# Performance work log

Measured on AMD Instinct MI355X. Metric: run time of the kernel, lower is better.

Reference implementation:

```python
import jax, jax.numpy as jnp
import numpy as np

B, C_IN, C_OUT, H, W, K = 8, 64, 64, 128, 128, 3
KK = K * K


def _conv(x, w, b):
    # 3x3, stride 1, padding 1 (matches nn.Conv2d(stride=1, padding=1))
    y = jax.lax.conv_general_dilated(
        x, w, window_strides=(1, 1), padding=((1, 1), (1, 1)),
        dimension_numbers=('NCHW', 'OIHW', 'NCHW'))
    return y + b[None, :, None, None]


def setup_inputs() -> dict:
    key = jax.random.key(0)
    k1, k2, k3, k4, k5 = jax.random.split(key, 5)
    x = jax.random.normal(k1, (B, C_IN, H, W), jnp.float32)
    s = 1.0 / np.sqrt(C_IN * K * K)  # torch conv default init range
    w_off = jax.random.uniform(k2, (2 * KK, C_IN, K, K), jnp.float32, -s, s)
    b_off = jax.random.uniform(k3, (2 * KK,), jnp.float32, -s, s)
    w_reg = jax.random.uniform(k4, (C_OUT, C_IN, K, K), jnp.float32, -s, s)
    b_reg = jax.random.uniform(k5, (C_OUT,), jnp.float32, -s, s)
    return {"x": x, "w_off": w_off, "b_off": b_off, "w_reg": w_reg, "b_reg": b_reg}


def _deform_sample(x, offsets):
    # Equivalent of the K*K grid_sample(align_corners=True, padding_mode='zeros')
    # loop + sum over kernel positions. The norm/unnorm cancel, so sampling is
    # at absolute pixel coords base_grid + offsets.
    B_, C, H_, W_ = x.shape
    off = offsets.reshape(B_, KK, 2, H_, W_).transpose(0, 3, 4, 1, 2)  # B,H,W,KK,2
    xs = off[..., 0] + jnp.arange(W_, dtype=x.dtype)[None, None, :, None]
    ys = off[..., 1] + jnp.arange(H_, dtype=x.dtype)[None, :, None, None]
    x0 = jnp.floor(xs)
    y0 = jnp.floor(ys)
    wx1 = xs - x0
    wx0 = 1.0 - wx1
    wy1 = ys - y0
    wy0 = 1.0 - wy1
    x_flat = x.reshape(B_, C, H_ * W_)

    def gather(yi, xi, w):
        valid = (xi >= 0) & (xi < W_) & (yi >= 0) & (yi < H_)  # zeros padding
        xi_c = jnp.clip(xi, 0, W_ - 1).astype(jnp.int32)
        yi_c = jnp.clip(yi, 0, H_ - 1).astype(jnp.int32)
        idx = (yi_c * W_ + xi_c).reshape(B_, 1, H_ * W_ * KK)
        g = jnp.take_along_axis(
            x_flat, jnp.broadcast_to(idx, (B_, C, H_ * W_ * KK)), axis=2)
        g = g.reshape(B_, C, H_, W_, KK)
        wm = (w * valid.astype(x.dtype))[:, None]  # B,1,H,W,KK
        return (g * wm).sum(-1)  # sum over the KK kernel positions

    return (gather(y0, x0, wy0 * wx0)
            + gather(y0, x0 + 1.0, wy0 * wx1)
            + gather(y0 + 1.0, x0, wy1 * wx0)
            + gather(y0 + 1.0, x0 + 1.0, wy1 * wx1))


def reference(x, w_off, b_off, w_reg, b_reg):
    offsets = _conv(x, w_off, b_off)          # B, 2*KK, H, W
    sampled = _deform_sample(x, offsets)      # B, C, H, W (summed over KK)
    return _conv(sampled, w_reg, b_reg)       # B, C_OUT, H, W
```

## Files before the change

### kernel.cpp

```cpp
#include <hip/hip_runtime.h>

#define B_ 8
#define CIN 64
#define COUT 64
#define H_ 128
#define W_ 128
#define HW (H_*W_)
#define OFFP 24

typedef __attribute__((ext_vector_type(8))) short short8;
typedef __attribute__((ext_vector_type(4))) short s16x4;
typedef __attribute__((ext_vector_type(4))) float f32x4;
typedef __attribute__((ext_vector_type(2))) float f32x2;

__device__ __forceinline__ short f2bf(float f) {
    unsigned u = __float_as_uint(f);
    unsigned r = (u + 0x7fffu + ((u >> 16) & 1u)) >> 16;
    return (short)r;
}
__device__ __forceinline__ float bf2f(short s) {
    return __uint_as_float(((unsigned)(unsigned short)s) << 16);
}

template<int NT>
__device__ __forceinline__ void prep_one(const float* __restrict__ w, short* __restrict__ o,
                                         int i, int n_used) {
    int j = i & 7, lane = (i >> 3) & 63, rest = i >> 9;
    int nt = rest % NT, dc = rest / NT, c = dc & 1, d = dc >> 1;
    int oc = nt * 16 + (lane & 15);
    int ic = c * 32 + (lane >> 4) * 8 + j;
    float v = (oc < n_used) ? w[(oc * 64 + ic) * 9 + d] : 0.f;
    o[i] = f2bf(v);
}

__global__ __launch_bounds__(256) void k_tr(const float* __restrict__ x,
                                            short* __restrict__ xt,
                                            const float* __restrict__ wof,
                                            const float* __restrict__ wrg,
                                            short* __restrict__ wt1,
                                            short* __restrict__ wt2) {
    int i = blockIdx.x * 256 + threadIdx.x;
    if (i < 9 * 2 * 2 * 512) prep_one<2>(wof, wt1, i, 18);
    if (i < 9 * 2 * 4 * 512) prep_one<4>(wrg, wt2, i, 64);

    __shared__ float tile[64 * 129];
    int bh = blockIdx.x;
    int bb = bh & 7, h = bh >> 3;
    const float* xp = x + (size_t)bb * (CIN * HW) + h * W_;
#pragma unroll
    for (int j = 0; j < 32; ++j) {
        int e = threadIdx.x + 256 * j;
        int cc = e >> 7, ww = e & 127;
        tile[cc * 129 + ww] = __builtin_nontemporal_load(xp + cc * HW + ww);
    }
    __syncthreads();
    short* op = xt + (((size_t)(bb << 7) + h) << 13);
#pragma unroll
    for (int j = 0; j < 4; ++j) {
        int t = threadIdx.x + 256 * j;
        int ww = t >> 3, c0 = (t & 7) << 3;
        short8 o;
#pragma unroll
        for (int k = 0; k < 8; ++k) o[k] = f2bf(tile[(c0 + k) * 129 + ww]);
        *(short8*)(op + ww * 64 + c0) = o;
    }
}

__device__ __forceinline__ void stage4(short* A, const short* __restrict__ src,
                                       int bb, int h0, int tid) {
    int wv = tid >> 6, l = tid & 63;
    int r = wv >> 1, half = wv & 1;
    int y = h0 - 1 + r;
    int P0 = 1 + half * 64;
    int px0 = P0 + (l >> 3);
    int ckl = l & 7;
    if ((unsigned)y < H_) {
        int ckg = ckl ^ (px0 & 7);
        const short* gp = src + ((((size_t)(bb << 7) + y) << 7) + (px0 - 1)) * 64 + ckg * 8;
#pragma unroll
        for (int i = 0; i < 8; ++i) {
            short* lp = &A[(r * 130 + P0 + i * 8) * 64];
            __builtin_amdgcn_global_load_lds(
                (const __attribute__((address_space(1))) void*)(gp + i * 512),
                (__attribute__((address_space(3))) void*)lp, 16, 0, 0);
        }
    } else {
        short8 z = {0, 0, 0, 0, 0, 0, 0, 0};
#pragma unroll
        for (int i = 0; i < 8; ++i)
            *(short8*)(&A[(r * 130 + P0 + i * 8) * 64 + l * 8]) = z;
    }
    if (tid < 64) {
        int rr = tid >> 4, side = (tid >> 3) & 1, ck = tid & 7;
        int px = side * 129;
        short8 z = {0, 0, 0, 0, 0, 0, 0, 0};
        *(short8*)(&A[(rr * 130 + px) * 64 + ((ck ^ (px & 7)) << 3)]) = z;
    }
}

__global__ __launch_bounds__(512, 4) void k_c1(const short* __restrict__ xt,
                                               const short* __restrict__ wt1,
                                               const float* __restrict__ bof,
                                               short* __restrict__ offb) {
    __shared__ __align__(16) short lds[33280 + 6144];
    short* A = lds;
    unsigned short* St = (unsigned short*)(lds + 33280);
    int blk = blockIdx.x, tid = threadIdx.x;
    int bb = blk & 7;
    int h0 = (blk >> 3) << 1;

    stage4(A, xt, bb, h0, tid);
    __syncthreads();

    int lane = tid & 63;
    int wave = tid >> 6;
    int lr = wave >> 2;
    int p0 = (wave & 3) * 32;
    int m = lane & 15, quad = lane >> 4;

    f32x4 acc[2][2];
#pragma unroll
    for (int nt = 0; nt < 2; ++nt) {
        int oc = nt * 16 + m;
        float bv = (oc < 18) ? bof[oc] : 0.f;
#pragma unroll
        for (int mt = 0; mt < 2; ++mt) {
            acc[mt][nt][0] = bv; acc[mt][nt][1] = bv;
            acc[mt][nt][2] = bv; acc[mt][nt][3] = bv;
        }
    }
#pragma unroll
    for (int d = 0; d < 9; ++d) {
        int dy = d / 3, dx = d % 3;
#pragma unroll
        for (int c = 0; c < 2; ++c) {
            short8 a[2];
#pragma unroll
            for (int mt = 0; mt < 2; ++mt) {
                int px = p0 + mt * 16 + m + dx;
                a[mt] = *(const short8*)(&A[((lr + dy) * 130 + px) * 64 + (((c * 4 + quad) ^ (px & 7)) << 3)]);
            }
#pragma unroll
            for (int nt = 0; nt < 2; ++nt) {
                short8 b = *(const short8*)(wt1 + ((((d * 2 + c) * 2 + nt) * 64 + lane) << 3));
#pragma unroll
                for (int mt = 0; mt < 2; ++mt)
                    acc[mt][nt] = __builtin_amdgcn_mfma_f32_16x16x32_bf16(a[mt], b, acc[mt][nt], 0, 0, 0);
            }
        }
    }
#pragma unroll
    for (int nt = 0; nt < 2; ++nt) {
        int oc = nt * 16 + m;
        if (oc < 18) {
#pragma unroll
            for (int mt = 0; mt < 2; ++mt) {
                int pl = lr * 128 + p0 + mt * 16 + quad * 4;
#pragma unroll
                for (int r = 0; r < 4; ++r)
                    St[(pl + r) * OFFP + oc] = (unsigned short)f2bf(acc[mt][nt][r]);
            }
        }
    }
    __syncthreads();
    const unsigned* Sd = (const unsigned*)St;
    unsigned* Od = (unsigned*)(offb + ((size_t)((bb << 14) + (h0 << 7))) * OFFP);
#pragma unroll
    for (int j = 0; j < 6; ++j)
        Od[tid + 512 * j] = Sd[tid + 512 * j];
}

__device__ __forceinline__ void prep_task_s(int t, int tw, int th,
                                            const unsigned* __restrict__ sow,
                                            s16x4* __restrict__ idxs,
                                            f32x4* __restrict__ wgs) {
    int px = (int)((unsigned)t / 9u);
    int tap = t - px * 9;
    int row = px >> 3, sx8 = px & 7;
    unsigned owk = sow[row * 96 + sx8 * 12 + tap];
    float ox = bf2f((short)(owk & 0xffff));
    float oy = bf2f((short)(owk >> 16));
    float xs = (float)((tw << 3) + sx8) + ox;
    float ys = (float)((th << 2) + row) + oy;
    float x0f = floorf(xs), y0f = floorf(ys);
    float wx1 = xs - x0f, wx0 = 1.f - wx1;
    float wy1 = ys - y0f, wy0 = 1.f - wy1;
    int x0 = (int)x0f, y0 = (int)y0f;
    int x1 = x0 + 1, y1 = y0 + 1;
    int x0c = min(max(x0, 0), W_ - 1), x1c = min(max(x1, 0), W_ - 1);
    int y0c = min(max(y0, 0), H_ - 1), y1c = min(max(y1, 0), H_ - 1);
    bool vx0 = ((unsigned)x0 < W_), vx1 = ((unsigned)x1 < W_);
    bool vy0 = ((unsigned)y0 < H_), vy1 = ((unsigned)y1 < H_);
    f32x4 wg;
    wg[0] = (vy0 && vx0) ? wy0 * wx0 : 0.f;
    wg[1] = (vy0 && vx1) ? wy0 * wx1 : 0.f;
    wg[2] = (vy1 && vx0) ? wy1 * wx0 : 0.f;
    wg[3] = (vy1 && vx1) ? wy1 * wx1 : 0.f;
    s16x4 id;
    id[0] = (short)(y0c * W_ + x0c);
    id[1] = (short)(y0c * W_ + x1c);
    id[2] = (short)(y1c * W_ + x0c);
    id[3] = (short)(y1c * W_ + x1c);
    idxs[t] = id;
    wgs[t] = wg;
}

__global__ __launch_bounds__(256, 4) void k_samp(const short* __restrict__ xt,
                                                 const short* __restrict__ offb,
                                                 short* __restrict__ smp) {
    __shared__ unsigned sow[4 * 96];
    __shared__ s16x4 idxs[288];
    __shared__ f32x4 wgs[288];
    int blk = blockIdx.x, tid = threadIdx.x;
    int bb = blk & 7;
    int tile = blk >> 3;
    int tw = tile & 15, th = tile >> 4;

    {
        int rowid = tid >> 6, rl = tid & 63;
        const unsigned* srcp = (const unsigned*)(offb +
            ((size_t)((bb << 14) + (((th << 2) + rowid) << 7) + (tw << 3))) * OFFP);
        sow[rowid * 96 + rl] = __builtin_nontemporal_load(srcp + rl);
        if (rl < 32) sow[rowid * 96 + 64 + rl] = __builtin_nontemporal_load(srcp + 64 + rl);
    }
    __syncthreads();

    prep_task_s(tid, tw, th, sow, idxs, wgs);
    if (tid < 32) prep_task_s(tid + 256, tw, th, sow, idxs, wgs);
    __syncthreads();

    int lp = tid >> 3, ck = tid & 7, cko = ck * 8;
    int w = (tw << 3) + (lp & 7);
    int h = (th << 2) + (lp >> 3);
    const short* ximc = xt + ((size_t)bb << 20) + cko;
    int pb = lp * 9;

    f32x2 acc2[4];
#pragma unroll
    for (int q = 0; q < 4; ++q) { acc2[q][0] = 0.f; acc2[q][1] = 0.f; }
#pragma unroll
    for (int g = 0; g < 3; ++g) {
        int eo[12]; float wf[12]; short8 v[12];
#pragma unroll
        for (int t2 = 0; t2 < 3; ++t2) {
            s16x4 id = idxs[pb + g * 3 + t2];
            f32x4 wv = wgs[pb + g * 3 + t2];
#pragma unroll
            for (int c = 0; c < 4; ++c) {
                eo[t2 * 4 + c] = ((int)id[c]) << 6;
                wf[t2 * 4 + c] = wv[c];
            }
        }
#pragma unroll
        for (int n = 0; n < 12; ++n) v[n] = *(const short8*)(ximc + eo[n]);
#pragma unroll
        for (int n = 0; n < 12; ++n) {
            float wvv = wf[n];
            f32x2 wp; wp[0] = wvv; wp[1] = wvv;
            const unsigned* vd = (const unsigned*)&v[n];
#pragma unroll
            for (int q = 0; q < 4; ++q) {
                unsigned dwd = vd[q];
                f32x2 av;
                av[0] = __uint_as_float(dwd << 16);
                av[1] = __uint_as_float(dwd & 0xffff0000u);
                asm("v_pk_fma_f32 %0, %1, %2, %0" : "+v"(acc2[q]) : "v"(av), "v"(wp));
            }
        }
    }
    short8 o;
#pragma unroll
    for (int i = 0; i < 8; ++i) o[i] = f2bf(acc2[i >> 1][i & 1]);
    *(short8*)(smp + ((((size_t)(bb << 7) + h) << 7) + w) * 64 + cko) = o;
}

__global__ __launch_bounds__(512, 4) void k_conv2(const short* __restrict__ smp,
                                                  const short* __restrict__ wt2,
                                                  const float* __restrict__ brg,
                                                  float* __restrict__ out) {
    __shared__ __align__(16) short A[4 * 130 * 64];
    int blk = blockIdx.x, tid = threadIdx.x;
    int bb = blk & 7;
    int h0 = (blk >> 3) << 1;

    stage4(A, smp, bb, h0, tid);
    __syncthreads();

    int lane = tid & 63;
    int wave = tid >> 6;
    int lr = wave >> 2;
    int p0 = (wave & 3) * 32;
    int m = lane & 15, quad = lane >> 4;

    f32x4 acc[2][4];
#pragma unroll
    for (int nt = 0; nt < 4; ++nt) {
        float bv = brg[nt * 16 + m];
#pragma unroll
        for (int mt = 0; mt < 2; ++mt) {
            acc[mt][nt][0] = bv; acc[mt][nt][1] = bv;
            acc[mt][nt][2] = bv; acc[mt][nt][3] = bv;
        }
    }
#pragma unroll
    for (int d = 0; d < 9; ++d) {
        int dy = d / 3, dx = d % 3;
#pragma unroll
        for (int c = 0; c < 2; ++c) {
            short8 a[2];
#pragma unroll
            for (int mt = 0; mt < 2; ++mt) {
                int px = p0 + mt * 16 + m + dx;
                a[mt] = *(const short8*)(&A[((lr + dy) * 130 + px) * 64 + (((c * 4 + quad) ^ (px & 7)) << 3)]);
            }
#pragma unroll
            for (int nt = 0; nt < 4; ++nt) {
                short8 b = *(const short8*)(wt2 + ((((d * 2 + c) * 4 + nt) * 64 + lane) << 3));
#pragma unroll
                for (int mt = 0; mt < 2; ++mt)
                    acc[mt][nt] = __builtin_amdgcn_mfma_f32_16x16x32_bf16(a[mt], b, acc[mt][nt], 0, 0, 0);
            }
        }
    }
#pragma unroll
    for (int nt = 0; nt < 4; ++nt) {
        int oc = nt * 16 + m;
#pragma unroll
        for (int mt = 0; mt < 2; ++mt) {
            int wpix = p0 + mt * 16 + quad * 4;
            __builtin_nontemporal_store(acc[mt][nt],
                (f32x4*)(out + (((size_t)(bb * 64 + oc)) << 14) + ((h0 + lr) << 7) + wpix));
        }
    }
}

extern "C" void kernel_launch(void* const* d_in, const int* in_sizes, int n_in,
                              void* d_out, int out_size, void* d_ws, size_t ws_size,
                              hipStream_t stream) {
    const float* x   = (const float*)d_in[0];
    const float* wof = (const float*)d_in[1];
    const float* bof = (const float*)d_in[2];
    const float* wrg = (const float*)d_in[3];
    const float* brg = (const float*)d_in[4];
    float* out = (float*)d_out;

    char* ws = (char*)d_ws;
    short* xt   = (short*)ws;
    short* smp  = (short*)(ws + 16777216);
    short* offb = (short*)(ws + 2 * 16777216);
    short* wt1  = (short*)(ws + 2 * 16777216 + 12582912);
    short* wt2  = (short*)(ws + 2 * 16777216 + 12582912 + 36864);

    k_tr   <<<dim3(B_ * H_),           256, 0, stream>>>(x, xt, wof, wrg, wt1, wt2);
    k_c1   <<<dim3(B_ * H_ / 2),       512, 0, stream>>>(xt, wt1, bof, offb);
    k_samp <<<dim3((B_ * HW) / 32),    256, 0, stream>>>(xt, offb, smp);
    k_conv2<<<dim3(B_ * H_ / 2),       512, 0, stream>>>(smp, wt2, brg, out);
}
```

Before: 144.3 us.

## Stage local input window in LDS for deformable sampling with global fallback

Before computing sample indices, the sampling kernel loads a 10x14-pixel x 64-channel haloed window of the input around each 4x8 tile into shared memory, using async global_load_lds with an XOR swizzle. Bilinear taps whose four corners fall inside the window read from LDS; the rest fall back to global gathers. This aims to replace scattered global gathers with LDS reads for the common case of small offsets. In exchange it adds about 20KB of LDS per block, which may reduce occupancy, adds a divergent branch, and gives up the previous batching of 12 loads in flight per group.

Result: slower. 149.4 us (+3.5%).

```diff
diff --git a/kernel.cpp b/kernel.cpp
--- a/kernel.cpp
+++ b/kernel.cpp
@@ -172,7 +172,8 @@
 
 __device__ __forceinline__ void prep_task_s(int t, int tw, int th,
                                             const unsigned* __restrict__ sow,
-                                            s16x4* __restrict__ idxs,
+                                            s16x4* __restrict__ idsL,
+                                            s16x4* __restrict__ idsG,
                                             f32x4* __restrict__ wgs) {
     int px = (int)((unsigned)t / 9u);
     int tap = t - px * 9;
@@ -196,21 +197,34 @@
     wg[1] = (vy0 && vx1) ? wy0 * wx1 : 0.f;
     wg[2] = (vy1 && vx0) ? wy1 * wx0 : 0.f;
     wg[3] = (vy1 && vx1) ? wy1 * wx1 : 0.f;
-    s16x4 id;
-    id[0] = (short)(y0c * W_ + x0c);
-    id[1] = (short)(y0c * W_ + x1c);
-    id[2] = (short)(y1c * W_ + x0c);
-    id[3] = (short)(y1c * W_ + x1c);
-    idxs[t] = id;
+    s16x4 idg;
+    idg[0] = (short)(y0c * W_ + x0c);
+    idg[1] = (short)(y0c * W_ + x1c);
+    idg[2] = (short)(y1c * W_ + x0c);
+    idg[3] = (short)(y1c * W_ + x1c);
+    idsG[t] = idg;
     wgs[t] = wg;
+    int wy = (th << 2) - 3, wx = (tw << 3) - 3;
+    int ly0 = y0c - wy, ly1 = y1c - wy;
+    int lx0 = x0c - wx, lx1 = x1c - wx;
+    bool inw = ((unsigned)ly0 < 10u) && ((unsigned)ly1 < 10u) &&
+               ((unsigned)lx0 < 14u) && ((unsigned)lx1 < 14u);
+    s16x4 idl;
+    idl[0] = (short)(inw ? (ly0 * 16 + lx0) : -1);
+    idl[1] = (short)(ly0 * 16 + lx1);
+    idl[2] = (short)(ly1 * 16 + lx0);
+    idl[3] = (short)(ly1 * 16 + lx1);
+    idsL[t] = idl;
 }
 
 __global__ __launch_bounds__(256, 4) void k_samp(const short* __restrict__ xt,
                                                  const short* __restrict__ offb,
                                                  short* __restrict__ smp) {
     __shared__ unsigned sow[4 * 96];
-    __shared__ s16x4 idxs[288];
+    __shared__ s16x4 idsL[288];
+    __shared__ s16x4 idsG[288];
     __shared__ f32x4 wgs[288];
+    __shared__ __align__(16) short win[10 * 16 * 64];
     int blk = blockIdx.x, tid = threadIdx.x;
     int bb = blk & 7;
     int tile = blk >> 3;
@@ -223,10 +237,32 @@
         sow[rowid * 96 + rl] = __builtin_nontemporal_load(srcp + rl);
         if (rl < 32) sow[rowid * 96 + 64 + rl] = __builtin_nontemporal_load(srcp + 64 + rl);
     }
-    __syncthreads();
-
-    prep_task_s(tid, tw, th, sow, idxs, wgs);
-    if (tid < 32) prep_task_s(tid + 256, tw, th, sow, idxs, wgs);
+
+    {
+        int wy = (th << 2) - 3, wx = (tw << 3) - 3;
+        const short* xim = xt + ((size_t)bb << 20);
+#pragma unroll
+        for (int it = 0; it < 5; ++it) {
+            int d = tid + 256 * it;
+            if (d < 1280) {
+                int ly = d >> 7, rem = d & 127, lx = rem >> 3, ckl = rem & 7;
+                if (lx < 14) {
+                    int gy = min(max(wy + ly, 0), H_ - 1);
+                    int gx = min(max(wx + lx, 0), W_ - 1);
+                    int ckg = ckl ^ (lx & 7);
+                    const short* gp = xim + (((size_t)gy << 7) + gx) * 64 + ckg * 8;
+                    short* lp = &win[((d & ~63)) * 8];
+                    __builtin_amdgcn_global_load_lds(
+                        (const __attribute__((address_space(1))) void*)gp,
+                        (__attribute__((address_space(3))) void*)lp, 16, 0, 0);
+                }
+            }
+        }
+    }
+    __syncthreads();
+
+    prep_task_s(tid, tw, th, sow, idsL, idsG, wgs);
+    if (tid < 32) prep_task_s(tid + 256, tw, th, sow, idsL, idsG, wgs);
     __syncthreads();
 
     int lp = tid >> 3, ck = tid & 7, cko = ck * 8;
@@ -239,25 +275,27 @@
 #pragma unroll
     for (int q = 0; q < 4; ++q) { acc2[q][0] = 0.f; acc2[q][1] = 0.f; }
 #pragma unroll
-    for (int g = 0; g < 3; ++g) {
-        int eo[12]; float wf[12]; short8 v[12];
-#pragma unroll
-        for (int t2 = 0; t2 < 3; ++t2) {
-            s16x4 id = idxs[pb + g * 3 + t2];
-            f32x4 wv = wgs[pb + g * 3 + t2];
+    for (int t = 0; t < 9; ++t) {
+        s16x4 idl = idsL[pb + t];
+        f32x4 wv = wgs[pb + t];
+        short8 v[4];
+        if (idl[0] >= 0) {
 #pragma unroll
             for (int c = 0; c < 4; ++c) {
-                eo[t2 * 4 + c] = ((int)id[c]) << 6;
-                wf[t2 * 4 + c] = wv[c];
-            }
-        }
-#pragma unroll
-        for (int n = 0; n < 12; ++n) v[n] = *(const short8*)(ximc + eo[n]);
-#pragma unroll
-        for (int n = 0; n < 12; ++n) {
-            float wvv = wf[n];
+                int pid = (int)idl[c];
+                v[c] = *(const short8*)(&win[pid * 64 + ((ck ^ (pid & 7)) << 3)]);
+            }
+        } else {
+            s16x4 idg = idsG[pb + t];
+#pragma unroll
+            for (int c = 0; c < 4; ++c)
+                v[c] = *(const short8*)(ximc + (((int)idg[c]) << 6));
+        }
+#pragma unroll
+        for (int c = 0; c < 4; ++c) {
+            float wvv = wv[c];
             f32x2 wp; wp[0] = wvv; wp[1] = wvv;
-            const unsigned* vd = (const unsigned*)&v[n];
+            const unsigned* vd = (const unsigned*)&v[c];
 #pragma unroll
             for (int q = 0; q < 4; ++q) {
                 unsigned dwd = vd[q];
```
